# Kernel optimization log

Hardware: AMD Instinct MI355X
Metric: run time of the kernel (lower is better)

## Reference

```python
import jax, jax.numpy as jnp
import numpy as np

TOP_K = 2
TEMP = 1.0

def setup_inputs() -> dict:
    key = jax.random.key(0)
    ks = jax.random.split(key, 7)
    B, T, D, E = 2, 2048, 768, 8
    F = 4 * D
    s = 0.02
    return {
        "x": jax.random.normal(ks[0], (B, T, D), dtype=jnp.float32),
        "gate_w": jax.random.normal(ks[1], (D, E), dtype=jnp.float32) * s,
        "gate_b": jnp.zeros((E,), dtype=jnp.float32),
        "w1": jax.random.normal(ks[2], (E, D, F), dtype=jnp.float32) * s,
        "b1": jnp.zeros((E, F), dtype=jnp.float32),
        "w2": jax.random.normal(ks[3], (E, F, D), dtype=jnp.float32) * s,
        "b2": jnp.zeros((E, D), dtype=jnp.float32),
    }

def reference(x, gate_w, gate_b, w1, b1, w2, b2):
    B, T, D = x.shape
    E = gate_w.shape[1]
    x_flat = x.reshape(-1, D)                       # [N, D]
    logits = x_flat @ gate_w + gate_b              # [N, E]
    gates = jax.nn.softmax(logits / TEMP, axis=-1)
    topk_gates, topk_idx = jax.lax.top_k(gates, TOP_K)   # [N, K]
    topk_gates = topk_gates / (jnp.sum(topk_gates, axis=-1, keepdims=True) + 1e-9)
    # Dense combine weights: w[n, e] = sum_k topk_gates[n, k] * (topk_idx[n, k] == e)
    combine = jnp.sum(
        topk_gates[:, :, None] * jax.nn.one_hot(topk_idx, E, dtype=x.dtype),
        axis=1,
    )                                               # [N, E]
    out = jnp.zeros_like(x_flat)
    for e in range(E):  # fixed small expert loop (structurally distinct params)
        h = jax.nn.gelu(x_flat @ w1[e] + b1[e], approximate=False)  # [N, 4D]
        y = h @ w2[e] + b2[e]                                       # [N, D]
        out = out + combine[:, e:e + 1] * y
    return out.reshape(B, T, D)
```

## Files before the change

kernel.cpp:

```cpp
#include <hip/hip_runtime.h>
#include <hip/hip_bf16.h>


#define N_TOK 4096
#define DIM   768
#define FDIM  3072
#define NEXP  8

typedef __attribute__((ext_vector_type(8))) _Float16 f16x8;
typedef __attribute__((ext_vector_type(4))) _Float16 f16x4;
typedef __attribute__((ext_vector_type(4))) float     f32x4;

__device__ __forceinline__ float gelu_exact(float v) {
    return 0.5f * v * (1.0f + erff(v * 0.7071067811865475f));
}

__device__ __forceinline__ void gload_lds16(const _Float16* g, _Float16* l) {
    __builtin_amdgcn_global_load_lds(
        (const __attribute__((address_space(1))) void*)g,
        (__attribute__((address_space(3))) void*)l,
        16, 0, 0);
}

__global__ __launch_bounds__(256) void cast_x_kernel(const float* __restrict__ x,
                                                     _Float16* __restrict__ xh) {
    int i = blockIdx.x * 256 + threadIdx.x;
    float4 v = ((const float4*)x)[i];
    f16x4 o;
    o[0] = (_Float16)v.x; o[1] = (_Float16)v.y;
    o[2] = (_Float16)v.z; o[3] = (_Float16)v.w;
    ((f16x4*)xh)[i] = o;
}

__global__ __launch_bounds__(256) void transpose_cast2_kernel(const float* __restrict__ w1,
                                                              const float* __restrict__ w2,
                                                              _Float16* __restrict__ w1t,
                                                              _Float16* __restrict__ w2t) {
    const int z     = blockIdx.y;
    const int which = z >> 3;
    const int e     = z & 7;
    const float* in; _Float16* out; int R, C, tx, ty;
    if (which == 0) { in = w1; out = w1t; R = DIM;  C = FDIM; tx = blockIdx.x % (FDIM / 64); ty = blockIdx.x / (FDIM / 64); }
    else            { in = w2; out = w2t; R = FDIM; C = DIM;  tx = blockIdx.x % (DIM  / 64); ty = blockIdx.x / (DIM  / 64); }
    const size_t eoff = (size_t)e * R * C;
    const int c0 = tx * 64;
    const int r0 = ty * 64;
    __shared__ _Float16 tile[64][66];
    const int t = threadIdx.x;
    #pragma unroll
    for (int it = 0; it < 4; it++) {
        int lin = it * 256 + t;
        int r  = lin >> 4;
        int c4 = lin & 15;
        float4 v = *(const float4*)&in[eoff + (size_t)(r0 + r) * C + c0 + c4 * 4];
        tile[r][c4 * 4 + 0] = (_Float16)v.x;
        tile[r][c4 * 4 + 1] = (_Float16)v.y;
        tile[r][c4 * 4 + 2] = (_Float16)v.z;
        tile[r][c4 * 4 + 3] = (_Float16)v.w;
    }
    __syncthreads();
    #pragma unroll
    for (int it = 0; it < 4; it++) {
        int lin = it * 256 + t;
        int c  = lin >> 4;
        int r4 = lin & 15;
        f16x4 o;
        #pragma unroll
        for (int j = 0; j < 4; j++) o[j] = tile[r4 * 4 + j][c];
        *(f16x4*)&out[eoff + (size_t)(c0 + c) * R + r0 + r4 * 4] = o;
    }
}

__global__ __launch_bounds__(256) void gate_kernel(const float* __restrict__ x,
                                                   const float* __restrict__ gw,
                                                   const float* __restrict__ gb,
                                                   int* __restrict__ tok_list,
                                                   float* __restrict__ wt_list,
                                                   int* __restrict__ count) {
    const int gtid = blockIdx.x * 256 + threadIdx.x;
    const int n    = gtid >> 6;
    const int lane = threadIdx.x & 63;
    if (n >= N_TOK) return;
    double part[NEXP];
    #pragma unroll
    for (int e = 0; e < NEXP; e++) part[e] = 0.0;
    for (int d = lane; d < DIM; d += 64) {
        float xv = x[n * DIM + d];
        const float* g = &gw[d * NEXP];
        #pragma unroll
        for (int e = 0; e < NEXP; e++) part[e] += (double)xv * (double)g[e];
    }
    #pragma unroll
    for (int e = 0; e < NEXP; e++) {
        double v = part[e];
        #pragma unroll
        for (int off = 32; off > 0; off >>= 1) v += __shfl_xor(v, off);
        part[e] = v + (double)gb[e];
    }
    if (lane == 0) {
        double mx = part[0];
        #pragma unroll
        for (int e = 1; e < NEXP; e++) mx = fmax(mx, part[e]);
        double ex[NEXP]; double s = 0.0;
        #pragma unroll
        for (int e = 0; e < NEXP; e++) { ex[e] = exp(part[e] - mx); s += ex[e]; }
        int i0 = 0;
        #pragma unroll
        for (int e = 1; e < NEXP; e++) if (ex[e] > ex[i0]) i0 = e;
        int i1 = (i0 == 0) ? 1 : 0;
        #pragma unroll
        for (int e = 0; e < NEXP; e++) if (e != i0 && ex[e] > ex[i1]) i1 = e;
        float g0 = (float)(ex[i0] / s), g1 = (float)(ex[i1] / s);
        float dn = g0 + g1 + 1e-9f;
        float w0 = g0 / dn, w1 = g1 / dn;
        int s0 = atomicAdd(&count[i0], 1);
        tok_list[i0 * N_TOK + s0] = n;  wt_list[i0 * N_TOK + s0] = w0;
        int s1 = atomicAdd(&count[i1], 1);
        tok_list[i1 * N_TOK + s1] = n;  wt_list[i1 * N_TOK + s1] = w1;
    }
}

__global__ void scan_kernel(const int* __restrict__ count, int* __restrict__ basep) {
    if (threadIdx.x == 0) {
        int s = 0;
        for (int e = 0; e < NEXP; e++) { basep[e] = s; s += count[e]; }
    }
}

__global__ __launch_bounds__(256) void mm1_kernel(const _Float16* __restrict__ xh,
                                                  const _Float16* __restrict__ w1t,
                                                  const float* __restrict__ bias1,
                                                  const int* __restrict__ tok_list,
                                                  const int* __restrict__ count,
                                                  const int* __restrict__ basep,
                                                  _Float16* __restrict__ h) {
    const int e    = blockIdx.y;
    const int cnt  = count[e];
    const int row0 = blockIdx.z * 128;
    if (row0 >= cnt) return;
    const int col0 = blockIdx.x * 128;
    const int t    = threadIdx.x;
    const int lane = t & 63;
    const int wv   = t >> 6;
    const int wy   = wv >> 1, wx = wv & 1;
    const int m_lane = lane & 15, quad = lane >> 4;

    __shared__ __align__(16) _Float16 As[128][64];
    __shared__ __align__(16) _Float16 Bs[128][64];

    const int srow = t >> 3;
    const int kin  = (t & 7) * 8;

    const _Float16* pa[4];
    #pragma unroll
    for (int g = 0; g < 4; g++) {
        int i = row0 + g * 32 + srow; if (i > cnt - 1) i = cnt - 1;
        pa[g] = xh + (size_t)tok_list[e * N_TOK + i] * DIM + kin;
    }
    const _Float16* pb[4];
    #pragma unroll
    for (int g = 0; g < 4; g++)
        pb[g] = w1t + (size_t)e * FDIM * DIM + (size_t)(col0 + g * 32 + srow) * DIM + kin;

    f32x4 acc[4][4];
    #pragma unroll
    for (int i = 0; i < 4; i++)
        #pragma unroll
        for (int j = 0; j < 4; j++)
            acc[i][j] = (f32x4){0.f, 0.f, 0.f, 0.f};

    for (int kk = 0; kk < DIM; kk += 64) {
        __syncthreads();
        #pragma unroll
        for (int g = 0; g < 4; g++) gload_lds16(pa[g] + kk, &As[g * 32 + srow][kin]);
        #pragma unroll
        for (int g = 0; g < 4; g++) gload_lds16(pb[g] + kk, &Bs[g * 32 + srow][kin]);
        __syncthreads();
        #pragma unroll
        for (int ks = 0; ks < 2; ks++) {
            f16x8 af[4], bf[4];
            #pragma unroll
            for (int i = 0; i < 4; i++)
                af[i] = *(const f16x8*)&As[wy * 64 + i * 16 + m_lane][ks * 32 + quad * 8];
            #pragma unroll
            for (int j = 0; j < 4; j++)
                bf[j] = *(const f16x8*)&Bs[wx * 64 + j * 16 + m_lane][ks * 32 + quad * 8];
            #pragma unroll
            for (int i = 0; i < 4; i++)
                #pragma unroll
                for (int j = 0; j < 4; j++)
                    acc[i][j] = __builtin_amdgcn_mfma_f32_16x16x32_f16(af[i], bf[j], acc[i][j], 0, 0, 0);
        }
    }

    const int hbase = basep[e];
    #pragma unroll
    for (int i = 0; i < 4; i++) {
        #pragma unroll
        for (int r = 0; r < 4; r++) {
            int rl = wy * 64 + i * 16 + quad * 4 + r;
            int gr = row0 + rl;
            if (gr < cnt) {
                _Float16* hrow = h + (size_t)(hbase + gr) * FDIM;
                #pragma unroll
                for (int j = 0; j < 4; j++) {
                    int c = col0 + wx * 64 + j * 16 + m_lane;
                    float v = acc[i][j][r] + bias1[e * FDIM + c];
                    hrow[c] = (_Float16)gelu_exact(v);
                }
            }
        }
    }
}

__global__ __launch_bounds__(256) void mm2_kernel(const _Float16* __restrict__ h,
                                                  const _Float16* __restrict__ w2t,
                                                  const float* __restrict__ bias2,
                                                  const int* __restrict__ tok_list,
                                                  const float* __restrict__ wt_list,
                                                  const int* __restrict__ count,
                                                  const int* __restrict__ basep,
                                                  float* __restrict__ out) {
    const int e    = blockIdx.y;
    const int cnt  = count[e];
    const int row0 = blockIdx.z * 64;
    if (row0 >= cnt) return;
    const int col0 = blockIdx.x * 128;
    const int t    = threadIdx.x;
    const int lane = t & 63;
    const int wv   = t >> 6;
    const int m_lane = lane & 15, quad = lane >> 4;

    __shared__ __align__(16) _Float16 As[64][64];
    __shared__ __align__(16) _Float16 Bs[128][64];

    const int srow = t >> 3;
    const int kin  = (t & 7) * 8;

    const int hbase = basep[e];
    const _Float16* pa[2];
    #pragma unroll
    for (int g = 0; g < 2; g++) {
        int i = row0 + g * 32 + srow; if (i > cnt - 1) i = cnt - 1;
        pa[g] = h + (size_t)(hbase + i) * FDIM + kin;
    }
    const _Float16* pb[4];
    #pragma unroll
    for (int g = 0; g < 4; g++)
        pb[g] = w2t + (size_t)e * DIM * FDIM + (size_t)(col0 + g * 32 + srow) * FDIM + kin;

    f32x4 acc[4][2];
    #pragma unroll
    for (int i = 0; i < 4; i++)
        #pragma unroll
        for (int j = 0; j < 2; j++)
            acc[i][j] = (f32x4){0.f, 0.f, 0.f, 0.f};

    for (int kk = 0; kk < FDIM; kk += 64) {
        __syncthreads();
        #pragma unroll
        for (int g = 0; g < 2; g++) gload_lds16(pa[g] + kk, &As[g * 32 + srow][kin]);
        #pragma unroll
        for (int g = 0; g < 4; g++) gload_lds16(pb[g] + kk, &Bs[g * 32 + srow][kin]);
        __syncthreads();
        #pragma unroll
        for (int ks = 0; ks < 2; ks++) {
            f16x8 af[4], bf[2];
            #pragma unroll
            for (int i = 0; i < 4; i++)
                af[i] = *(const f16x8*)&As[i * 16 + m_lane][ks * 32 + quad * 8];
            #pragma unroll
            for (int j = 0; j < 2; j++)
                bf[j] = *(const f16x8*)&Bs[wv * 32 + j * 16 + m_lane][ks * 32 + quad * 8];
            #pragma unroll
            for (int i = 0; i < 4; i++)
                #pragma unroll
                for (int j = 0; j < 2; j++)
                    acc[i][j] = __builtin_amdgcn_mfma_f32_16x16x32_f16(af[i], bf[j], acc[i][j], 0, 0, 0);
        }
    }

    #pragma unroll
    for (int i = 0; i < 4; i++) {
        #pragma unroll
        for (int r = 0; r < 4; r++) {
            int rl = i * 16 + quad * 4 + r;
            int gr = row0 + rl;
            if (gr < cnt) {
                int tok   = tok_list[e * N_TOK + gr];
                float wgt = wt_list[e * N_TOK + gr];
                float* orow = out + (size_t)tok * DIM;
                #pragma unroll
                for (int j = 0; j < 2; j++) {
                    int c = col0 + wv * 32 + j * 16 + m_lane;
                    float v = acc[i][j][r] + bias2[e * DIM + c];
                    atomicAdd(&orow[c], wgt * v);
                }
            }
        }
    }
}

extern "C" void kernel_launch(void* const* d_in, const int* in_sizes, int n_in,
                              void* d_out, int out_size, void* d_ws, size_t ws_size,
                              hipStream_t stream) {
    const float* x  = (const float*)d_in[0];
    const float* gw = (const float*)d_in[1];
    const float* gb = (const float*)d_in[2];
    const float* w1 = (const float*)d_in[3];
    const float* b1 = (const float*)d_in[4];
    const float* w2 = (const float*)d_in[5];
    const float* b2 = (const float*)d_in[6];
    float* out = (float*)d_out;

    char* ws = (char*)d_ws;
    _Float16* xh   = (_Float16*)ws;
    _Float16* w1t  = xh  + (size_t)N_TOK * DIM;
    _Float16* w2t  = w1t + (size_t)NEXP * FDIM * DIM;
    _Float16* hbuf = w2t + (size_t)NEXP * DIM * FDIM;
    int*   tok_list = (int*)(hbuf + (size_t)2 * N_TOK * FDIM);
    float* wt_list  = (float*)(tok_list + NEXP * N_TOK);
    int*   count    = (int*)(wt_list + NEXP * N_TOK);
    int*   basep    = count + 8;

    hipMemsetAsync(count, 0, 64, stream);
    hipMemsetAsync(out, 0, (size_t)out_size * sizeof(float), stream);

    cast_x_kernel<<<dim3(N_TOK * DIM / 4 / 256), 256, 0, stream>>>(x, xh);
    transpose_cast2_kernel<<<dim3(576, 16), 256, 0, stream>>>(w1, w2, w1t, w2t);
    gate_kernel<<<dim3(N_TOK / 4), 256, 0, stream>>>(x, gw, gb, tok_list, wt_list, count);
    scan_kernel<<<1, 64, 0, stream>>>(count, basep);
    mm1_kernel<<<dim3(FDIM / 128, NEXP, N_TOK / 128), 256, 0, stream>>>(
        xh, w1t, b1, tok_list, count, basep, hbuf);
    mm2_kernel<<<dim3(DIM / 128, NEXP, N_TOK / 64), 256, 0, stream>>>(
        hbuf, w2t, b2, tok_list, wt_list, count, basep, out);
}
```

Measured before the change: 506.9 us.

## Triple-buffer LDS with async loads and XOR swizzle in expert GEMMs

Both expert GEMM kernels switch from a single LDS buffer with two full syncthreads per 64-wide K step to a three-stage ring of 32-wide K tiles. Global-to-LDS loads for later tiles are issued ahead and gated with explicit vmcnt waits and raw barriers, so memory latency can overlap MFMA work. Source columns are XOR-swizzled to reduce LDS bank conflicts. MFMA operands are swapped so each lane holds four consecutive output columns, which allows vectorized bias loads and f16x4 stores of h. The hand-counted vmcnt values are fragile and depend on the exact number of outstanding loads per stage.

```diff
diff --git a/kernel.cpp b/kernel.cpp
--- a/kernel.cpp
+++ b/kernel.cpp
@@ -21,6 +21,9 @@
         (__attribute__((address_space(3))) void*)l,
         16, 0, 0);
 }
+
+#define WAITV(N) asm volatile("s_waitcnt vmcnt(" #N ")" ::: "memory")
+#define BAR()    __builtin_amdgcn_s_barrier()
 
 __global__ __launch_bounds__(256) void cast_x_kernel(const float* __restrict__ x,
                                                      _Float16* __restrict__ xh) {
@@ -145,22 +148,19 @@
     const int wy   = wv >> 1, wx = wv & 1;
     const int m_lane = lane & 15, quad = lane >> 4;
 
-    __shared__ __align__(16) _Float16 As[128][64];
-    __shared__ __align__(16) _Float16 Bs[128][64];
-
-    const int srow = t >> 3;
-    const int kin  = (t & 7) * 8;
-
-    const _Float16* pa[4];
-    #pragma unroll
-    for (int g = 0; g < 4; g++) {
-        int i = row0 + g * 32 + srow; if (i > cnt - 1) i = cnt - 1;
-        pa[g] = xh + (size_t)tok_list[e * N_TOK + i] * DIM + kin;
-    }
-    const _Float16* pb[4];
-    #pragma unroll
-    for (int g = 0; g < 4; g++)
-        pb[g] = w1t + (size_t)e * FDIM * DIM + (size_t)(col0 + g * 32 + srow) * DIM + kin;
+    __shared__ __align__(16) _Float16 A0[128][32], A1[128][32], A2[128][32];
+    __shared__ __align__(16) _Float16 B0[128][32], B1[128][32], B2[128][32];
+
+    const int srow    = t >> 2;
+    const int kin     = (t & 3) * 8;
+    const int kin_src = ((t & 3) ^ ((srow >> 1) & 3)) * 8;
+
+    int i0 = row0 + srow;      if (i0 > cnt - 1) i0 = cnt - 1;
+    int i1 = row0 + 64 + srow; if (i1 > cnt - 1) i1 = cnt - 1;
+    const _Float16* pa0 = xh + (size_t)tok_list[e * N_TOK + i0] * DIM + kin_src;
+    const _Float16* pa1 = xh + (size_t)tok_list[e * N_TOK + i1] * DIM + kin_src;
+    const _Float16* pb0 = w1t + (size_t)e * FDIM * DIM + (size_t)(col0 + srow) * DIM + kin_src;
+    const _Float16* pb1 = pb0 + (size_t)64 * DIM;
 
     f32x4 acc[4][4];
     #pragma unroll
@@ -169,48 +169,56 @@
         for (int j = 0; j < 4; j++)
             acc[i][j] = (f32x4){0.f, 0.f, 0.f, 0.f};
 
-    for (int kk = 0; kk < DIM; kk += 64) {
-        __syncthreads();
-        #pragma unroll
-        for (int g = 0; g < 4; g++) gload_lds16(pa[g] + kk, &As[g * 32 + srow][kin]);
-        #pragma unroll
-        for (int g = 0; g < 4; g++) gload_lds16(pb[g] + kk, &Bs[g * 32 + srow][kin]);
-        __syncthreads();
-        #pragma unroll
-        for (int ks = 0; ks < 2; ks++) {
-            f16x8 af[4], bf[4];
+    const int rc8 = (quad ^ ((m_lane >> 1) & 3)) * 8;
+
+#define MM1_STAGE(Ad, Bd, kt) do { const int kk_ = (kt) * 32;          \
+    gload_lds16(pa0 + kk_, &Ad[srow][kin]);                             \
+    gload_lds16(pa1 + kk_, &Ad[64 + srow][kin]);                        \
+    gload_lds16(pb0 + kk_, &Bd[srow][kin]);                             \
+    gload_lds16(pb1 + kk_, &Bd[64 + srow][kin]); } while (0)
+
+#define MM1_COMP(Ac, Bc) do { f16x8 af_[4], bf_[4];                                         \
+    _Pragma("unroll") for (int i_ = 0; i_ < 4; i_++)                                        \
+        af_[i_] = *(const f16x8*)&Ac[wy * 64 + i_ * 16 + m_lane][rc8];                      \
+    _Pragma("unroll") for (int j_ = 0; j_ < 4; j_++)                                        \
+        bf_[j_] = *(const f16x8*)&Bc[wx * 64 + j_ * 16 + m_lane][rc8];                      \
+    _Pragma("unroll") for (int i_ = 0; i_ < 4; i_++)                                        \
+        _Pragma("unroll") for (int j_ = 0; j_ < 4; j_++)                                    \
+            acc[i_][j_] = __builtin_amdgcn_mfma_f32_16x16x32_f16(bf_[j_], af_[i_], acc[i_][j_], 0, 0, 0); } while (0)
+
+    WAITV(0);
+    MM1_STAGE(A0, B0, 0);
+    MM1_STAGE(A1, B1, 1);
+    for (int tt = 0; tt < 21; tt += 3) {
+        MM1_STAGE(A2, B2, tt + 2); WAITV(8); BAR(); MM1_COMP(A0, B0); BAR();
+        MM1_STAGE(A0, B0, tt + 3); WAITV(8); BAR(); MM1_COMP(A1, B1); BAR();
+        MM1_STAGE(A1, B1, tt + 4); WAITV(8); BAR(); MM1_COMP(A2, B2); BAR();
+    }
+    MM1_STAGE(A2, B2, 23); WAITV(8); BAR(); MM1_COMP(A0, B0); BAR();
+    WAITV(4); BAR(); MM1_COMP(A1, B1); BAR();
+    WAITV(0); BAR(); MM1_COMP(A2, B2);
+
+    const int hbase = basep[e];
+    #pragma unroll
+    for (int i = 0; i < 4; i++) {
+        int gr = row0 + wy * 64 + i * 16 + m_lane;
+        if (gr < cnt) {
+            _Float16* hrow = h + (size_t)(hbase + gr) * FDIM;
             #pragma unroll
-            for (int i = 0; i < 4; i++)
-                af[i] = *(const f16x8*)&As[wy * 64 + i * 16 + m_lane][ks * 32 + quad * 8];
-            #pragma unroll
-            for (int j = 0; j < 4; j++)
-                bf[j] = *(const f16x8*)&Bs[wx * 64 + j * 16 + m_lane][ks * 32 + quad * 8];
-            #pragma unroll
-            for (int i = 0; i < 4; i++)
-                #pragma unroll
-                for (int j = 0; j < 4; j++)
-                    acc[i][j] = __builtin_amdgcn_mfma_f32_16x16x32_f16(af[i], bf[j], acc[i][j], 0, 0, 0);
-        }
-    }
-
-    const int hbase = basep[e];
-    #pragma unroll
-    for (int i = 0; i < 4; i++) {
-        #pragma unroll
-        for (int r = 0; r < 4; r++) {
-            int rl = wy * 64 + i * 16 + quad * 4 + r;
-            int gr = row0 + rl;
-            if (gr < cnt) {
-                _Float16* hrow = h + (size_t)(hbase + gr) * FDIM;
-                #pragma unroll
-                for (int j = 0; j < 4; j++) {
-                    int c = col0 + wx * 64 + j * 16 + m_lane;
-                    float v = acc[i][j][r] + bias1[e * FDIM + c];
-                    hrow[c] = (_Float16)gelu_exact(v);
-                }
+            for (int j = 0; j < 4; j++) {
+                int c = col0 + wx * 64 + j * 16 + quad * 4;
+                float4 b4 = *(const float4*)&bias1[e * FDIM + c];
+                f16x4 o;
+                o[0] = (_Float16)gelu_exact(acc[i][j][0] + b4.x);
+                o[1] = (_Float16)gelu_exact(acc[i][j][1] + b4.y);
+                o[2] = (_Float16)gelu_exact(acc[i][j][2] + b4.z);
+                o[3] = (_Float16)gelu_exact(acc[i][j][3] + b4.w);
+                *(f16x4*)&hrow[c] = o;
             }
         }
     }
+#undef MM1_STAGE
+#undef MM1_COMP
 }
 
 __global__ __launch_bounds__(256) void mm2_kernel(const _Float16* __restrict__ h,
@@ -231,23 +239,18 @@
     const int wv   = t >> 6;
     const int m_lane = lane & 15, quad = lane >> 4;
 
-    __shared__ __align__(16) _Float16 As[64][64];
-    __shared__ __align__(16) _Float16 Bs[128][64];
-
-    const int srow = t >> 3;
-    const int kin  = (t & 7) * 8;
+    __shared__ __align__(16) _Float16 A0[64][32],  A1[64][32],  A2[64][32];
+    __shared__ __align__(16) _Float16 B0[128][32], B1[128][32], B2[128][32];
+
+    const int srow    = t >> 2;
+    const int kin     = (t & 3) * 8;
+    const int kin_src = ((t & 3) ^ ((srow >> 1) & 3)) * 8;
 
     const int hbase = basep[e];
-    const _Float16* pa[2];
-    #pragma unroll
-    for (int g = 0; g < 2; g++) {
-        int i = row0 + g * 32 + srow; if (i > cnt - 1) i = cnt - 1;
-        pa[g] = h + (size_t)(hbase + i) * FDIM + kin;
-    }
-    const _Float16* pb[4];
-    #pragma unroll
-    for (int g = 0; g < 4; g++)
-        pb[g] = w2t + (size_t)e * DIM * FDIM + (size_t)(col0 + g * 32 + srow) * FDIM + kin;
+    int ia = row0 + srow; if (ia > cnt - 1) ia = cnt - 1;
+    const _Float16* pa  = h + (size_t)(hbase + ia) * FDIM + kin_src;
+    const _Float16* pb0 = w2t + (size_t)e * DIM * FDIM + (size_t)(col0 + srow) * FDIM + kin_src;
+    const _Float16* pb1 = pb0 + (size_t)64 * FDIM;
 
     f32x4 acc[4][2];
     #pragma unroll
@@ -256,49 +259,54 @@
         for (int j = 0; j < 2; j++)
             acc[i][j] = (f32x4){0.f, 0.f, 0.f, 0.f};
 
-    for (int kk = 0; kk < FDIM; kk += 64) {
-        __syncthreads();
-        #pragma unroll
-        for (int g = 0; g < 2; g++) gload_lds16(pa[g] + kk, &As[g * 32 + srow][kin]);
-        #pragma unroll
-        for (int g = 0; g < 4; g++) gload_lds16(pb[g] + kk, &Bs[g * 32 + srow][kin]);
-        __syncthreads();
-        #pragma unroll
-        for (int ks = 0; ks < 2; ks++) {
-            f16x8 af[4], bf[2];
+    const int rc8 = (quad ^ ((m_lane >> 1) & 3)) * 8;
+
+#define MM2_STAGE(Ad, Bd, kt) do { const int kk_ = (kt) * 32;          \
+    gload_lds16(pa  + kk_, &Ad[srow][kin]);                             \
+    gload_lds16(pb0 + kk_, &Bd[srow][kin]);                             \
+    gload_lds16(pb1 + kk_, &Bd[64 + srow][kin]); } while (0)
+
+#define MM2_COMP(Ac, Bc) do { f16x8 af_[4], bf_[2];                                         \
+    _Pragma("unroll") for (int i_ = 0; i_ < 4; i_++)                                        \
+        af_[i_] = *(const f16x8*)&Ac[i_ * 16 + m_lane][rc8];                                \
+    _Pragma("unroll") for (int j_ = 0; j_ < 2; j_++)                                        \
+        bf_[j_] = *(const f16x8*)&Bc[wv * 32 + j_ * 16 + m_lane][rc8];                      \
+    _Pragma("unroll") for (int i_ = 0; i_ < 4; i_++)                                        \
+        _Pragma("unroll") for (int j_ = 0; j_ < 2; j_++)                                    \
+            acc[i_][j_] = __builtin_amdgcn_mfma_f32_16x16x32_f16(bf_[j_], af_[i_], acc[i_][j_], 0, 0, 0); } while (0)
+
+    WAITV(0);
+    MM2_STAGE(A0, B0, 0);
+    MM2_STAGE(A1, B1, 1);
+    for (int tt = 0; tt < 93; tt += 3) {
+        MM2_STAGE(A2, B2, tt + 2); WAITV(6); BAR(); MM2_COMP(A0, B0); BAR();
+        MM2_STAGE(A0, B0, tt + 3); WAITV(6); BAR(); MM2_COMP(A1, B1); BAR();
+        MM2_STAGE(A1, B1, tt + 4); WAITV(6); BAR(); MM2_COMP(A2, B2); BAR();
+    }
+    MM2_STAGE(A2, B2, 95); WAITV(6); BAR(); MM2_COMP(A0, B0); BAR();
+    WAITV(3); BAR(); MM2_COMP(A1, B1); BAR();
+    WAITV(0); BAR(); MM2_COMP(A2, B2);
+
+    #pragma unroll
+    for (int i = 0; i < 4; i++) {
+        int gr = row0 + i * 16 + m_lane;
+        if (gr < cnt) {
+            int tok   = tok_list[e * N_TOK + gr];
+            float wgt = wt_list[e * N_TOK + gr];
+            float* orow = out + (size_t)tok * DIM;
             #pragma unroll
-            for (int i = 0; i < 4; i++)
-                af[i] = *(const f16x8*)&As[i * 16 + m_lane][ks * 32 + quad * 8];
-            #pragma unroll
-            for (int j = 0; j < 2; j++)
-                bf[j] = *(const f16x8*)&Bs[wv * 32 + j * 16 + m_lane][ks * 32 + quad * 8];
-            #pragma unroll
-            for (int i = 0; i < 4; i++)
-                #pragma unroll
-                for (int j = 0; j < 2; j++)
-                    acc[i][j] = __builtin_amdgcn_mfma_f32_16x16x32_f16(af[i], bf[j], acc[i][j], 0, 0, 0);
-        }
-    }
-
-    #pragma unroll
-    for (int i = 0; i < 4; i++) {
-        #pragma unroll
-        for (int r = 0; r < 4; r++) {
-            int rl = i * 16 + quad * 4 + r;
-            int gr = row0 + rl;
-            if (gr < cnt) {
-                int tok   = tok_list[e * N_TOK + gr];
-                float wgt = wt_list[e * N_TOK + gr];
-                float* orow = out + (size_t)tok * DIM;
-                #pragma unroll
-                for (int j = 0; j < 2; j++) {
-                    int c = col0 + wv * 32 + j * 16 + m_lane;
-                    float v = acc[i][j][r] + bias2[e * DIM + c];
-                    atomicAdd(&orow[c], wgt * v);
-                }
+            for (int j = 0; j < 2; j++) {
+                int c = col0 + wv * 32 + j * 16 + quad * 4;
+                float4 b4 = *(const float4*)&bias2[e * DIM + c];
+                atomicAdd(&orow[c + 0], wgt * (acc[i][j][0] + b4.x));
+                atomicAdd(&orow[c + 1], wgt * (acc[i][j][1] + b4.y));
+                atomicAdd(&orow[c + 2], wgt * (acc[i][j][2] + b4.z));
+                atomicAdd(&orow[c + 3], wgt * (acc[i][j][3] + b4.w));
             }
         }
     }
+#undef MM2_STAGE
+#undef MM2_COMP
 }
 
 extern "C" void kernel_launch(void* const* d_in, const int* in_sizes, int n_in,
```

New measurement: 544.8 us. 1.07x slower.

## Drop LDS staging in expert GEMMs; load MFMA fragments directly from global

Applied to the files above, without the earlier changes.

Both expert GEMM kernels stop staging A and B tiles through shared memory with global_load_lds and barriers. Each lane now loads its MFMA operand fragments straight from global memory (relying on L1/L2 for reuse across waves). The mm1 operand order is swapped so accumulators hold four consecutive columns, which allows vectorized bias loads and f16x4 stores of the GELU output. mm2 changes its wave layout to 2x2. This removes barrier and LDS traffic but duplicates global loads across waves and loses explicit data reuse, so it risks becoming bound by cache bandwidth.

```diff
diff --git a/kernel.cpp b/kernel.cpp
--- a/kernel.cpp
+++ b/kernel.cpp
@@ -13,13 +13,6 @@
 
 __device__ __forceinline__ float gelu_exact(float v) {
     return 0.5f * v * (1.0f + erff(v * 0.7071067811865475f));
-}
-
-__device__ __forceinline__ void gload_lds16(const _Float16* g, _Float16* l) {
-    __builtin_amdgcn_global_load_lds(
-        (const __attribute__((address_space(1))) void*)g,
-        (__attribute__((address_space(3))) void*)l,
-        16, 0, 0);
 }
 
 __global__ __launch_bounds__(256) void cast_x_kernel(const float* __restrict__ x,
@@ -145,22 +138,17 @@
     const int wy   = wv >> 1, wx = wv & 1;
     const int m_lane = lane & 15, quad = lane >> 4;
 
-    __shared__ __align__(16) _Float16 As[128][64];
-    __shared__ __align__(16) _Float16 Bs[128][64];
-
-    const int srow = t >> 3;
-    const int kin  = (t & 7) * 8;
-
-    const _Float16* pa[4];
-    #pragma unroll
-    for (int g = 0; g < 4; g++) {
-        int i = row0 + g * 32 + srow; if (i > cnt - 1) i = cnt - 1;
-        pa[g] = xh + (size_t)tok_list[e * N_TOK + i] * DIM + kin;
-    }
-    const _Float16* pb[4];
-    #pragma unroll
-    for (int g = 0; g < 4; g++)
-        pb[g] = w1t + (size_t)e * FDIM * DIM + (size_t)(col0 + g * 32 + srow) * DIM + kin;
+    const _Float16* pA[4];
+    #pragma unroll
+    for (int i = 0; i < 4; i++) {
+        int r = row0 + wy * 64 + i * 16 + m_lane; if (r > cnt - 1) r = cnt - 1;
+        pA[i] = xh + (size_t)tok_list[e * N_TOK + r] * DIM + quad * 8;
+    }
+    const _Float16* pB[4];
+    #pragma unroll
+    for (int j = 0; j < 4; j++)
+        pB[j] = w1t + (size_t)e * FDIM * DIM
+                    + (size_t)(col0 + wx * 64 + j * 16 + m_lane) * DIM + quad * 8;
 
     f32x4 acc[4][4];
     #pragma unroll
@@ -169,45 +157,36 @@
         for (int j = 0; j < 4; j++)
             acc[i][j] = (f32x4){0.f, 0.f, 0.f, 0.f};
 
-    for (int kk = 0; kk < DIM; kk += 64) {
-        __syncthreads();
-        #pragma unroll
-        for (int g = 0; g < 4; g++) gload_lds16(pa[g] + kk, &As[g * 32 + srow][kin]);
-        #pragma unroll
-        for (int g = 0; g < 4; g++) gload_lds16(pb[g] + kk, &Bs[g * 32 + srow][kin]);
-        __syncthreads();
-        #pragma unroll
-        for (int ks = 0; ks < 2; ks++) {
-            f16x8 af[4], bf[4];
-            #pragma unroll
-            for (int i = 0; i < 4; i++)
-                af[i] = *(const f16x8*)&As[wy * 64 + i * 16 + m_lane][ks * 32 + quad * 8];
+    #pragma unroll 4
+    for (int kk = 0; kk < DIM; kk += 32) {
+        f16x8 af[4], bf[4];
+        #pragma unroll
+        for (int i = 0; i < 4; i++) af[i] = *(const f16x8*)(pA[i] + kk);
+        #pragma unroll
+        for (int j = 0; j < 4; j++) bf[j] = *(const f16x8*)(pB[j] + kk);
+        #pragma unroll
+        for (int i = 0; i < 4; i++)
             #pragma unroll
             for (int j = 0; j < 4; j++)
-                bf[j] = *(const f16x8*)&Bs[wx * 64 + j * 16 + m_lane][ks * 32 + quad * 8];
+                acc[i][j] = __builtin_amdgcn_mfma_f32_16x16x32_f16(bf[j], af[i], acc[i][j], 0, 0, 0);
+    }
+
+    const int hbase = basep[e];
+    #pragma unroll
+    for (int i = 0; i < 4; i++) {
+        int gr = row0 + wy * 64 + i * 16 + m_lane;
+        if (gr < cnt) {
+            _Float16* hrow = h + (size_t)(hbase + gr) * FDIM;
             #pragma unroll
-            for (int i = 0; i < 4; i++)
-                #pragma unroll
-                for (int j = 0; j < 4; j++)
-                    acc[i][j] = __builtin_amdgcn_mfma_f32_16x16x32_f16(af[i], bf[j], acc[i][j], 0, 0, 0);
-        }
-    }
-
-    const int hbase = basep[e];
-    #pragma unroll
-    for (int i = 0; i < 4; i++) {
-        #pragma unroll
-        for (int r = 0; r < 4; r++) {
-            int rl = wy * 64 + i * 16 + quad * 4 + r;
-            int gr = row0 + rl;
-            if (gr < cnt) {
-                _Float16* hrow = h + (size_t)(hbase + gr) * FDIM;
-                #pragma unroll
-                for (int j = 0; j < 4; j++) {
-                    int c = col0 + wx * 64 + j * 16 + m_lane;
-                    float v = acc[i][j][r] + bias1[e * FDIM + c];
-                    hrow[c] = (_Float16)gelu_exact(v);
-                }
+            for (int j = 0; j < 4; j++) {
+                int c = col0 + wx * 64 + j * 16 + quad * 4;
+                float4 b4 = *(const float4*)&bias1[e * FDIM + c];
+                f16x4 o;
+                o[0] = (_Float16)gelu_exact(acc[i][j][0] + b4.x);
+                o[1] = (_Float16)gelu_exact(acc[i][j][1] + b4.y);
+                o[2] = (_Float16)gelu_exact(acc[i][j][2] + b4.z);
+                o[3] = (_Float16)gelu_exact(acc[i][j][3] + b4.w);
+                *(f16x4*)&hrow[c] = o;
             }
         }
     }
@@ -229,70 +208,55 @@
     const int t    = threadIdx.x;
     const int lane = t & 63;
     const int wv   = t >> 6;
+    const int wy   = wv >> 1, wx = wv & 1;
     const int m_lane = lane & 15, quad = lane >> 4;
 
-    __shared__ __align__(16) _Float16 As[64][64];
-    __shared__ __align__(16) _Float16 Bs[128][64];
-
-    const int srow = t >> 3;
-    const int kin  = (t & 7) * 8;
-
     const int hbase = basep[e];
-    const _Float16* pa[2];
-    #pragma unroll
-    for (int g = 0; g < 2; g++) {
-        int i = row0 + g * 32 + srow; if (i > cnt - 1) i = cnt - 1;
-        pa[g] = h + (size_t)(hbase + i) * FDIM + kin;
-    }
-    const _Float16* pb[4];
-    #pragma unroll
-    for (int g = 0; g < 4; g++)
-        pb[g] = w2t + (size_t)e * DIM * FDIM + (size_t)(col0 + g * 32 + srow) * FDIM + kin;
-
-    f32x4 acc[4][2];
-    #pragma unroll
-    for (int i = 0; i < 4; i++)
-        #pragma unroll
-        for (int j = 0; j < 2; j++)
+    const _Float16* pA[2];
+    #pragma unroll
+    for (int i = 0; i < 2; i++) {
+        int r = row0 + wy * 32 + i * 16 + m_lane; if (r > cnt - 1) r = cnt - 1;
+        pA[i] = h + (size_t)(hbase + r) * FDIM + quad * 8;
+    }
+    const _Float16* pB[4];
+    #pragma unroll
+    for (int j = 0; j < 4; j++)
+        pB[j] = w2t + (size_t)e * DIM * FDIM
+                    + (size_t)(col0 + wx * 64 + j * 16 + m_lane) * FDIM + quad * 8;
+
+    f32x4 acc[2][4];
+    #pragma unroll
+    for (int i = 0; i < 2; i++)
+        #pragma unroll
+        for (int j = 0; j < 4; j++)
             acc[i][j] = (f32x4){0.f, 0.f, 0.f, 0.f};
 
-    for (int kk = 0; kk < FDIM; kk += 64) {
-        __syncthreads();
-        #pragma unroll
-        for (int g = 0; g < 2; g++) gload_lds16(pa[g] + kk, &As[g * 32 + srow][kin]);
-        #pragma unroll
-        for (int g = 0; g < 4; g++) gload_lds16(pb[g] + kk, &Bs[g * 32 + srow][kin]);
-        __syncthreads();
-        #pragma unroll
-        for (int ks = 0; ks < 2; ks++) {
-            f16x8 af[4], bf[2];
+    #pragma unroll 4
+    for (int kk = 0; kk < FDIM; kk += 32) {
+        f16x8 af[2], bf[4];
+        #pragma unroll
+        for (int i = 0; i < 2; i++) af[i] = *(const f16x8*)(pA[i] + kk);
+        #pragma unroll
+        for (int j = 0; j < 4; j++) bf[j] = *(const f16x8*)(pB[j] + kk);
+        #pragma unroll
+        for (int i = 0; i < 2; i++)
             #pragma unroll
-            for (int i = 0; i < 4; i++)
-                af[i] = *(const f16x8*)&As[i * 16 + m_lane][ks * 32 + quad * 8];
-            #pragma unroll
-            for (int j = 0; j < 2; j++)
-                bf[j] = *(const f16x8*)&Bs[wv * 32 + j * 16 + m_lane][ks * 32 + quad * 8];
-            #pragma unroll
-            for (int i = 0; i < 4; i++)
-                #pragma unroll
-                for (int j = 0; j < 2; j++)
-                    acc[i][j] = __builtin_amdgcn_mfma_f32_16x16x32_f16(af[i], bf[j], acc[i][j], 0, 0, 0);
-        }
-    }
-
-    #pragma unroll
-    for (int i = 0; i < 4; i++) {
+            for (int j = 0; j < 4; j++)
+                acc[i][j] = __builtin_amdgcn_mfma_f32_16x16x32_f16(af[i], bf[j], acc[i][j], 0, 0, 0);
+    }
+
+    #pragma unroll
+    for (int i = 0; i < 2; i++) {
         #pragma unroll
         for (int r = 0; r < 4; r++) {
-            int rl = i * 16 + quad * 4 + r;
-            int gr = row0 + rl;
+            int gr = row0 + wy * 32 + i * 16 + quad * 4 + r;
             if (gr < cnt) {
                 int tok   = tok_list[e * N_TOK + gr];
                 float wgt = wt_list[e * N_TOK + gr];
                 float* orow = out + (size_t)tok * DIM;
                 #pragma unroll
-                for (int j = 0; j < 2; j++) {
-                    int c = col0 + wv * 32 + j * 16 + m_lane;
+                for (int j = 0; j < 4; j++) {
+                    int c = col0 + wx * 64 + j * 16 + m_lane;
                     float v = acc[i][j][r] + bias2[e * DIM + c];
                     atomicAdd(&orow[c], wgt * v);
                 }
```

Result: slower. 752.0 us (+48.3%).
